# Kernel tuning notes

Hardware: AMD Instinct MI355X
Metric: run time of the kernel (lower is better)

The kernel has to match this reference:

```python
import jax, jax.numpy as jnp
import numpy as np

B, C, H, W = 4, 64, 64, 64
CQK = C // 4  # query/key channels = in_dim // 4


def setup_inputs() -> dict:
    key = jax.random.key(0)
    ks = jax.random.split(key, 9)
    s = 0.05
    return {
        "x": jax.random.normal(ks[0], (B, C, H, W), jnp.float32),
        "x_RGB": jax.random.normal(ks[1], (B, C, H, W), jnp.float32),
        "Wq": jax.random.normal(ks[2], (CQK, C), jnp.float32) * s,  # 1x1 conv weight
        "bq": jax.random.normal(ks[3], (CQK,), jnp.float32) * s,
        "Wk": jax.random.normal(ks[4], (CQK, C), jnp.float32) * s,
        "bk": jax.random.normal(ks[5], (CQK,), jnp.float32) * s,
        "Wv": jax.random.normal(ks[6], (C, C), jnp.float32) * s,
        "bv": jax.random.normal(ks[7], (C,), jnp.float32) * s,
        "lam": jnp.zeros((1,), jnp.float32) + 0.5,  # nn.Parameter init is 0; use 0.5 so output depends on attention
    }


def reference(x, x_RGB, Wq, bq, Wk, bk, Wv, bv, lam):
    b, c, h, w = x.shape
    n = h * w
    xf = x.reshape(b, c, n)          # B,C,N
    xr = x_RGB.reshape(b, c, n)      # B,C,N
    # 1x1 convs are channel matmuls
    q = jnp.einsum('oc,bcn->bno', Wq, xr) + bq            # B,N,Cqk  (permuted query)
    k = jnp.einsum('oc,bcn->bon', Wk, xf) + bk[:, None]   # B,Cqk,N
    v = jnp.einsum('oc,bcn->bon', Wv, xf) + bv[:, None]   # B,C,N
    energy = jnp.einsum('bio,boj->bij', q, k)             # B,N,N
    attention = jax.nn.softmax(energy, axis=-1)
    # out[b,c,i] = sum_j V[b,c,j] * attention[b,i,j]
    out = jnp.einsum('bcj,bij->bci', v, attention)        # B,C,N
    out = out.reshape(b, c, h, w)
    return lam[0] * out + x
```

## Files before the change

### kernel.cpp

```cpp
#include <hip/hip_runtime.h>
#include <hip/hip_bf16.h>
#include <math.h>

#define B_   4
#define C_   64
#define N_   4096
#define L2E  1.4426950408889634f

typedef __attribute__((ext_vector_type(8)))  short bf16x8;
typedef __attribute__((ext_vector_type(4)))  float f32x4;
typedef __attribute__((ext_vector_type(16))) float f32x16;
typedef __attribute__((ext_vector_type(4)))  uint  uint4v;

#define MFMA16(a,b,c) __builtin_amdgcn_mfma_f32_16x16x32_bf16(a,b,c,0,0,0)
#define MFMA32(a,b,c) __builtin_amdgcn_mfma_f32_32x32x16_bf16(a,b,c,0,0,0)

static __device__ inline ushort f2bf(float f) {
    __hip_bfloat16 h = __float2bfloat16(f);
    return *reinterpret_cast<ushort*>(&h);
}
static __device__ inline uint packbf(float a, float b) {
    return (uint)f2bf(a) | ((uint)f2bf(b) << 16);
}
static __device__ inline uint cvtpk(float lo, float hi) {
    uint r;
    asm("v_cvt_pk_bf16_f32 %0, %1, %2" : "=v"(r) : "v"(lo), "v"(hi));
    return r;
}
static __device__ inline void plswap(uint &a, uint &b) {
    asm("v_permlane32_swap_b32 %0, %1" : "+v"(a), "+v"(b));
}
static __device__ inline float tmax16(const f32x16 &s) {
    float a0 = fmaxf(s[0], s[1]),  a1 = fmaxf(s[2], s[3]);
    float a2 = fmaxf(s[4], s[5]),  a3 = fmaxf(s[6], s[7]);
    float a4 = fmaxf(s[8], s[9]),  a5 = fmaxf(s[10], s[11]);
    float a6 = fmaxf(s[12], s[13]), a7 = fmaxf(s[14], s[15]);
    a0 = fmaxf(a0, a1); a2 = fmaxf(a2, a3); a4 = fmaxf(a4, a5); a6 = fmaxf(a6, a7);
    return fmaxf(fmaxf(a0, a2), fmaxf(a4, a6));
}
static __device__ inline float tsum16(const f32x16 &s) {
    float a0 = s[0] + s[1],  a1 = s[2] + s[3];
    float a2 = s[4] + s[5],  a3 = s[6] + s[7];
    float a4 = s[8] + s[9],  a5 = s[10] + s[11];
    float a6 = s[12] + s[13], a7 = s[14] + s[15];
    a0 += a1; a2 += a3; a4 += a5; a6 += a7;
    return (a0 + a2) + (a4 + a6);
}

__global__ __launch_bounds__(256) void qkv_mfma(
    const float* __restrict__ x, const float* __restrict__ xrgb,
    const float* __restrict__ Wq, const float* __restrict__ bq,
    const float* __restrict__ Wk, const float* __restrict__ bk,
    const float* __restrict__ Wv, const float* __restrict__ bv,
    ushort* __restrict__ Qo, ushort* __restrict__ Ko, ushort* __restrict__ Vo)
{
    __shared__ float BLs[96];
    __shared__ float OP[2][96][33];

    const int t = threadIdx.x, b = blockIdx.y, n0 = blockIdx.x * 32;
    const int w = t >> 6, lane = t & 63, li = lane & 15, g = lane >> 4;
    const int pw = w & 1, cw = w >> 1;

    const int n = n0 + pw * 16 + li;
    const int c0 = cw * 32 + g * 8;
    const float* xb = x    + ((size_t)b * C_ + c0) * N_ + n;
    const float* rb = xrgb + ((size_t)b * C_ + c0) * N_ + n;
    float fx[8], fr[8];
    #pragma unroll
    for (int r = 0; r < 8; ++r) { fx[r] = xb[(size_t)r * N_]; fr[r] = rb[(size_t)r * N_]; }

    float wf[6][8];
    #pragma unroll
    for (int ot = 0; ot < 6; ++ot) {
        const float* wsrc;
        if (ot == 0)      wsrc = Wq + li * 64 + c0;
        else if (ot == 1) wsrc = Wk + li * 64 + c0;
        else              wsrc = Wv + ((ot - 2) * 16 + li) * 64 + c0;
        const float4 a = *(const float4*)(wsrc);
        const float4 c = *(const float4*)(wsrc + 4);
        wf[ot][0] = a.x; wf[ot][1] = a.y; wf[ot][2] = a.z; wf[ot][3] = a.w;
        wf[ot][4] = c.x; wf[ot][5] = c.y; wf[ot][6] = c.z; wf[ot][7] = c.w;
    }

    if (t < 96)
        BLs[t] = (t < 16) ? bq[t] * L2E : (t < 32 ? bk[t - 16] : bv[t - 32]);

    bf16x8 bxf, brf;
    #pragma unroll
    for (int r = 0; r < 8; ++r) {
        bxf[r] = (short)f2bf(fx[r]);
        brf[r] = (short)f2bf(fr[r]);
    }

    const f32x4 cz = {0.f, 0.f, 0.f, 0.f};
    #pragma unroll
    for (int ot = 0; ot < 6; ++ot) {
        bf16x8 wa;
        const float s = (ot == 0) ? L2E : 1.0f;
        #pragma unroll
        for (int r = 0; r < 8; ++r) wa[r] = (short)f2bf(wf[ot][r] * s);
        const f32x4 acc = MFMA16(wa, (ot == 0 ? brf : bxf), cz);
        #pragma unroll
        for (int r = 0; r < 4; ++r)
            OP[cw][ot * 16 + g * 4 + r][pw * 16 + li] = acc[r];
    }
    __syncthreads();

    {
        const int p = t >> 3, cp = t & 7;
        const float q0 = OP[0][cp * 2][p]     + OP[1][cp * 2][p]     + BLs[cp * 2];
        const float q1 = OP[0][cp * 2 + 1][p] + OP[1][cp * 2 + 1][p] + BLs[cp * 2 + 1];
        *(uint*)&Qo[(size_t)(b * N_ + n0 + p) * 16 + cp * 2] = packbf(q0, q1);
        const float k0 = OP[0][16 + cp * 2][p]     + OP[1][16 + cp * 2][p]     + BLs[16 + cp * 2];
        const float k1 = OP[0][16 + cp * 2 + 1][p] + OP[1][16 + cp * 2 + 1][p] + BLs[16 + cp * 2 + 1];
        *(uint*)&Ko[(size_t)(b * N_ + n0 + p) * 16 + cp * 2] = packbf(k0, k1);
    }
    {
        const int ch = t >> 2, po = (t & 3) * 8;
        const float bs = BLs[32 + ch];
        uint4 o;
        #pragma unroll
        for (int e = 0; e < 4; ++e) {
            const float v0 = OP[0][32 + ch][po + 2 * e]     + OP[1][32 + ch][po + 2 * e]     + bs;
            const float v1 = OP[0][32 + ch][po + 2 * e + 1] + OP[1][32 + ch][po + 2 * e + 1] + bs;
            ((uint*)&o)[e] = packbf(v0, v1);
        }
        const size_t jt = (size_t)b * (N_ / 16) + ((n0 + po) >> 4);
        *(uint4*)&Vo[(jt * 64 + ch) * 16 + (po & 8)] = o;
    }
}

#define JG_   8
#define OTP   36
#define SMEM_FL (73728 + 1056 + 1056 + 128)

__global__ __launch_bounds__(512, 4) void flash32(
    const ushort* __restrict__ Qg, const ushort* __restrict__ Kg,
    const ushort* __restrict__ VT, const float* __restrict__ x,
    const float* __restrict__ lam, float* __restrict__ out)
{
    __shared__ __align__(16) char smem[SMEM_FL];
    float*  OT = (float*)smem;
    float*  MC = (float*)(smem + 73728);
    float*  LC = (float*)(smem + 73728 + 1056);
    float*  IV = (float*)(smem + 73728 + 2112);

    const int t = threadIdx.x, w = t >> 6, lane = t & 63;
    const int l31 = lane & 31, h = lane >> 5;

    const int wg = blockIdx.x;
    const int b  = (wg & 7) >> 1;
    const int it = ((wg >> 3) << 1) | (wg & 1);
    const int i0 = it * 32;

    const bf16x8 qf = *(const bf16x8*)(Qg + ((size_t)(b * N_ + i0 + l31)) * 16 + h * 8);

    const size_t jbase = (size_t)w * (N_ / JG_);
    const ushort* kp = Kg + ((size_t)(b * N_) + jbase + l31) * 16 + h * 8;
    const ushort* vt = VT + (((size_t)b * (N_ / 16) + jbase / 16) * 64 + l31) * 16 + h * 8;

    f32x16 acc0, acc1, z16;
    #pragma unroll
    for (int i = 0; i < 16; ++i) { acc0[i] = 0.f; acc1[i] = 0.f; z16[i] = 0.f; }
    float m_run = -1e30f, l_loc = 0.f;

    #pragma unroll 1
    for (int it8 = 0; it8 < 8; ++it8) {
        const int j0 = it8 * 64;

        const bf16x8 kf0 = *(const bf16x8*)(kp + (size_t)(j0) * 16);
        const bf16x8 kf1 = *(const bf16x8*)(kp + (size_t)(j0 + 32) * 16);
        f32x16 st0 = MFMA32(kf0, qf, z16);
        f32x16 st1 = MFMA32(kf1, qf, z16);

        float m_c = fmaxf(tmax16(st0), tmax16(st1));
        m_c = fmaxf(m_c, __shfl_xor(m_c, 32));
        if (__any(m_c > m_run + 8.f)) {
            const float m_new = fmaxf(m_run, m_c);
            const float sc = exp2f(m_run - m_new);
            l_loc *= sc;
            #pragma unroll
            for (int i = 0; i < 16; ++i) { acc0[i] *= sc; acc1[i] *= sc; }
            m_run = m_new;
        }
        #pragma unroll
        for (int i = 0; i < 16; ++i) st0[i] = exp2f(st0[i] - m_run);
        #pragma unroll
        for (int i = 0; i < 16; ++i) st1[i] = exp2f(st1[i] - m_run);
        l_loc += tsum16(st0) + tsum16(st1);

        uint A0 = cvtpk(st0[0],  st0[1]),  A1 = cvtpk(st0[2],  st0[3]);
        uint B0 = cvtpk(st0[4],  st0[5]),  B1 = cvtpk(st0[6],  st0[7]);
        uint C0 = cvtpk(st0[8],  st0[9]),  C1 = cvtpk(st0[10], st0[11]);
        uint D0 = cvtpk(st0[12], st0[13]), D1 = cvtpk(st0[14], st0[15]);
        plswap(A0, B0); plswap(A1, B1); plswap(C0, D0); plswap(C1, D1);
        uint E0 = cvtpk(st1[0],  st1[1]),  E1 = cvtpk(st1[2],  st1[3]);
        uint F0 = cvtpk(st1[4],  st1[5]),  F1 = cvtpk(st1[6],  st1[7]);
        uint G0 = cvtpk(st1[8],  st1[9]),  G1 = cvtpk(st1[10], st1[11]);
        uint H0 = cvtpk(st1[12], st1[13]), H1 = cvtpk(st1[14], st1[15]);
        plswap(E0, F0); plswap(E1, F1); plswap(G0, H0); plswap(G1, H1);
        uint4v u0 = {A0, A1, B0, B1}, u1 = {C0, C1, D0, D1};
        uint4v u2 = {E0, E1, F0, F1}, u3 = {G0, G1, H0, H1};
        const bf16x8 pf0 = __builtin_bit_cast(bf16x8, u0);
        const bf16x8 pf1 = __builtin_bit_cast(bf16x8, u1);
        const bf16x8 pf2 = __builtin_bit_cast(bf16x8, u2);
        const bf16x8 pf3 = __builtin_bit_cast(bf16x8, u3);

        const ushort* vtj = vt + (size_t)(j0 >> 4) * 1024;
        const bf16x8 va0 = *(const bf16x8*)(vtj);
        const bf16x8 va1 = *(const bf16x8*)(vtj + 1024);
        const bf16x8 va2 = *(const bf16x8*)(vtj + 2048);
        const bf16x8 va3 = *(const bf16x8*)(vtj + 3072);
        acc0 = MFMA32(va0, pf0, acc0);
        acc0 = MFMA32(va1, pf1, acc0);
        acc0 = MFMA32(va2, pf2, acc0);
        acc0 = MFMA32(va3, pf3, acc0);
        const bf16x8 vb0 = *(const bf16x8*)(vtj + 512);
        const bf16x8 vb1 = *(const bf16x8*)(vtj + 1536);
        const bf16x8 vb2 = *(const bf16x8*)(vtj + 2560);
        const bf16x8 vb3 = *(const bf16x8*)(vtj + 3584);
        acc1 = MFMA32(vb0, pf0, acc1);
        acc1 = MFMA32(vb1, pf1, acc1);
        acc1 = MFMA32(vb2, pf2, acc1);
        acc1 = MFMA32(vb3, pf3, acc1);
    }
    const float l_run = l_loc + __shfl_xor(l_loc, 32);

    if (h == 0) { MC[w * 33 + l31] = m_run; LC[w * 33 + l31] = l_run; }
    __syncthreads();

    float mp[8];
    #pragma unroll
    for (int p = 0; p < 8; ++p) mp[p] = MC[p * 33 + l31];
    float ms = mp[0];
    #pragma unroll
    for (int p = 1; p < 8; ++p) ms = fmaxf(ms, mp[p]);
    float lsum = 0.f, wt_own = 0.f;
    #pragma unroll
    for (int p = 0; p < 8; ++p) {
        const float wt = exp2f(mp[p] - ms);
        lsum += wt * LC[p * 33 + l31];
        if (p == w) wt_own = wt;
    }
    if (w == 0 && h == 0) IV[l31] = lam[0] / lsum;

    #pragma unroll
    for (int r = 0; r < 16; ++r) {
        const int c = (r & 3) + 8 * (r >> 2) + 4 * h;
        OT[(w * 64 + c) * OTP + l31]      = acc0[r] * wt_own;
        OT[(w * 64 + c + 32) * OTP + l31] = acc1[r] * wt_own;
    }
    __syncthreads();

    {
        const int c = t >> 3, sg = t & 7;
        f32x4 o = {0.f, 0.f, 0.f, 0.f};
        #pragma unroll
        for (int p = 0; p < 8; ++p) {
            const f32x4 v = *(const f32x4*)&OT[(p * 64 + c) * OTP + sg * 4];
            o[0] += v[0]; o[1] += v[1]; o[2] += v[2]; o[3] += v[3];
        }
        const size_t off = ((size_t)b * C_ + c) * N_ + i0 + sg * 4;
        const float4 xv = *(const float4*)(x + off);
        float4 res;
        res.x = o[0] * IV[sg * 4 + 0] + xv.x;
        res.y = o[1] * IV[sg * 4 + 1] + xv.y;
        res.z = o[2] * IV[sg * 4 + 2] + xv.z;
        res.w = o[3] * IV[sg * 4 + 3] + xv.w;
        *(float4*)(out + off) = res;
    }
}

extern "C" void kernel_launch(void* const* d_in, const int* in_sizes, int n_in,
                              void* d_out, int out_size, void* d_ws, size_t ws_size,
                              hipStream_t stream)
{
    (void)in_sizes; (void)n_in; (void)out_size; (void)ws_size;
    const float* x    = (const float*)d_in[0];
    const float* xrgb = (const float*)d_in[1];
    const float* Wq   = (const float*)d_in[2];
    const float* bq   = (const float*)d_in[3];
    const float* Wk   = (const float*)d_in[4];
    const float* bk   = (const float*)d_in[5];
    const float* Wv   = (const float*)d_in[6];
    const float* bv   = (const float*)d_in[7];
    const float* lam  = (const float*)d_in[8];
    float* out = (float*)d_out;

    ushort* Qw = (ushort*)d_ws;
    ushort* Kw = Qw + (size_t)B_ * N_ * 16;
    ushort* Vw = Kw + (size_t)B_ * N_ * 16;

    qkv_mfma<<<dim3(N_ / 32, B_), 256, 0, stream>>>(
        x, xrgb, Wq, bq, Wk, bk, Wv, bv, Qw, Kw, Vw);

    flash32<<<dim3(512), 512, 0, stream>>>(
        Qw, Kw, Vw, x, lam, out);
}
```

Measured before the change: 36.80 us.

## Drop LDS reduction in QKV projection and shrink flash loop tile to 32 keys

The projection kernel now has each wave accumulate over both channel halves with chained MFMAs and write bias-added bf16 results straight to global memory. This removes the shared-memory partial-sum buffers and the block barrier. The V output becomes scattered 2-byte stores instead of 16-byte vector stores. The attention kernel processes 32 keys per iteration instead of 64, which halves live score registers and interleaves the two accumulator chains, at the cost of twice as many iterations and more frequent max checks.

```diff
diff --git a/kernel.cpp b/kernel.cpp
--- a/kernel.cpp
+++ b/kernel.cpp
@@ -54,79 +54,66 @@
     const float* __restrict__ Wv, const float* __restrict__ bv,
     ushort* __restrict__ Qo, ushort* __restrict__ Ko, ushort* __restrict__ Vo)
 {
-    __shared__ float BLs[96];
-    __shared__ float OP[2][96][33];
-
     const int t = threadIdx.x, b = blockIdx.y, n0 = blockIdx.x * 32;
     const int w = t >> 6, lane = t & 63, li = lane & 15, g = lane >> 4;
-    const int pw = w & 1, cw = w >> 1;
-
-    const int n = n0 + pw * 16 + li;
-    const int c0 = cw * 32 + g * 8;
-    const float* xb = x    + ((size_t)b * C_ + c0) * N_ + n;
-    const float* rb = xrgb + ((size_t)b * C_ + c0) * N_ + n;
-    float fx[8], fr[8];
-    #pragma unroll
-    for (int r = 0; r < 8; ++r) { fx[r] = xb[(size_t)r * N_]; fr[r] = rb[(size_t)r * N_]; }
-
-    float wf[6][8];
-    #pragma unroll
-    for (int ot = 0; ot < 6; ++ot) {
+    const int pw = w & 1, oh = w >> 1;
+
+    const int px = n0 + pw * 16 + li;
+
+    bf16x8 bxf[2], brf[2];
+    #pragma unroll
+    for (int kk = 0; kk < 2; ++kk) {
+        const int c0 = kk * 32 + g * 8;
+        const float* xb = x + ((size_t)b * C_ + c0) * N_ + px;
+        #pragma unroll
+        for (int r = 0; r < 8; ++r) bxf[kk][r] = (short)f2bf(xb[(size_t)r * N_]);
+        if (oh == 0) {
+            const float* rb = xrgb + ((size_t)b * C_ + c0) * N_ + px;
+            #pragma unroll
+            for (int r = 0; r < 8; ++r) brf[kk][r] = (short)f2bf(rb[(size_t)r * N_]);
+        }
+    }
+
+    const f32x4 cz = {0.f, 0.f, 0.f, 0.f};
+    #pragma unroll
+    for (int j = 0; j < 3; ++j) {
+        const int ot = oh * 3 + j;
         const float* wsrc;
-        if (ot == 0)      wsrc = Wq + li * 64 + c0;
-        else if (ot == 1) wsrc = Wk + li * 64 + c0;
-        else              wsrc = Wv + ((ot - 2) * 16 + li) * 64 + c0;
-        const float4 a = *(const float4*)(wsrc);
-        const float4 c = *(const float4*)(wsrc + 4);
-        wf[ot][0] = a.x; wf[ot][1] = a.y; wf[ot][2] = a.z; wf[ot][3] = a.w;
-        wf[ot][4] = c.x; wf[ot][5] = c.y; wf[ot][6] = c.z; wf[ot][7] = c.w;
-    }
-
-    if (t < 96)
-        BLs[t] = (t < 16) ? bq[t] * L2E : (t < 32 ? bk[t - 16] : bv[t - 32]);
-
-    bf16x8 bxf, brf;
-    #pragma unroll
-    for (int r = 0; r < 8; ++r) {
-        bxf[r] = (short)f2bf(fx[r]);
-        brf[r] = (short)f2bf(fr[r]);
-    }
-
-    const f32x4 cz = {0.f, 0.f, 0.f, 0.f};
-    #pragma unroll
-    for (int ot = 0; ot < 6; ++ot) {
-        bf16x8 wa;
+        const float* bsrc;
+        if (ot == 0)      { wsrc = Wq + li * 64;              bsrc = bq; }
+        else if (ot == 1) { wsrc = Wk + li * 64;              bsrc = bk; }
+        else              { wsrc = Wv + ((ot - 2) * 16 + li) * 64; bsrc = bv + (ot - 2) * 16; }
         const float s = (ot == 0) ? L2E : 1.0f;
-        #pragma unroll
-        for (int r = 0; r < 8; ++r) wa[r] = (short)f2bf(wf[ot][r] * s);
-        const f32x4 acc = MFMA16(wa, (ot == 0 ? brf : bxf), cz);
-        #pragma unroll
-        for (int r = 0; r < 4; ++r)
-            OP[cw][ot * 16 + g * 4 + r][pw * 16 + li] = acc[r];
-    }
-    __syncthreads();
-
-    {
-        const int p = t >> 3, cp = t & 7;
-        const float q0 = OP[0][cp * 2][p]     + OP[1][cp * 2][p]     + BLs[cp * 2];
-        const float q1 = OP[0][cp * 2 + 1][p] + OP[1][cp * 2 + 1][p] + BLs[cp * 2 + 1];
-        *(uint*)&Qo[(size_t)(b * N_ + n0 + p) * 16 + cp * 2] = packbf(q0, q1);
-        const float k0 = OP[0][16 + cp * 2][p]     + OP[1][16 + cp * 2][p]     + BLs[16 + cp * 2];
-        const float k1 = OP[0][16 + cp * 2 + 1][p] + OP[1][16 + cp * 2 + 1][p] + BLs[16 + cp * 2 + 1];
-        *(uint*)&Ko[(size_t)(b * N_ + n0 + p) * 16 + cp * 2] = packbf(k0, k1);
-    }
-    {
-        const int ch = t >> 2, po = (t & 3) * 8;
-        const float bs = BLs[32 + ch];
-        uint4 o;
-        #pragma unroll
-        for (int e = 0; e < 4; ++e) {
-            const float v0 = OP[0][32 + ch][po + 2 * e]     + OP[1][32 + ch][po + 2 * e]     + bs;
-            const float v1 = OP[0][32 + ch][po + 2 * e + 1] + OP[1][32 + ch][po + 2 * e + 1] + bs;
-            ((uint*)&o)[e] = packbf(v0, v1);
-        }
-        const size_t jt = (size_t)b * (N_ / 16) + ((n0 + po) >> 4);
-        *(uint4*)&Vo[(jt * 64 + ch) * 16 + (po & 8)] = o;
+
+        f32x4 acc = cz;
+        #pragma unroll
+        for (int kk = 0; kk < 2; ++kk) {
+            const int c0 = kk * 32 + g * 8;
+            const float4 a  = *(const float4*)(wsrc + c0);
+            const float4 c4 = *(const float4*)(wsrc + c0 + 4);
+            bf16x8 wa;
+            wa[0] = (short)f2bf(a.x * s);  wa[1] = (short)f2bf(a.y * s);
+            wa[2] = (short)f2bf(a.z * s);  wa[3] = (short)f2bf(a.w * s);
+            wa[4] = (short)f2bf(c4.x * s); wa[5] = (short)f2bf(c4.y * s);
+            wa[6] = (short)f2bf(c4.z * s); wa[7] = (short)f2bf(c4.w * s);
+            acc = MFMA16(wa, (ot == 0 ? brf[kk] : bxf[kk]), acc);
+        }
+        const float b0 = bsrc[g * 4 + 0] * s, b1 = bsrc[g * 4 + 1] * s;
+        const float b2 = bsrc[g * 4 + 2] * s, b3 = bsrc[g * 4 + 3] * s;
+        if (ot < 2) {
+            uint2 pwd;
+            pwd.x = packbf(acc[0] + b0, acc[1] + b1);
+            pwd.y = packbf(acc[2] + b2, acc[3] + b3);
+            ushort* dst = (ot == 0 ? Qo : Ko) + (size_t)(b * N_ + px) * 16 + g * 4;
+            *(uint2*)dst = pwd;
+        } else {
+            const size_t base = (((size_t)b * (N_ / 16) + (px >> 4)) * 64
+                                 + (ot - 2) * 16 + g * 4) * 16 + (px & 15);
+            Vo[base]      = f2bf(acc[0] + b0);
+            Vo[base + 16] = f2bf(acc[1] + b1);
+            Vo[base + 32] = f2bf(acc[2] + b2);
+            Vo[base + 48] = f2bf(acc[3] + b3);
+        }
     }
 }
 
@@ -165,15 +152,11 @@
     float m_run = -1e30f, l_loc = 0.f;
 
     #pragma unroll 1
-    for (int it8 = 0; it8 < 8; ++it8) {
-        const int j0 = it8 * 64;
-
-        const bf16x8 kf0 = *(const bf16x8*)(kp + (size_t)(j0) * 16);
-        const bf16x8 kf1 = *(const bf16x8*)(kp + (size_t)(j0 + 32) * 16);
-        f32x16 st0 = MFMA32(kf0, qf, z16);
-        f32x16 st1 = MFMA32(kf1, qf, z16);
-
-        float m_c = fmaxf(tmax16(st0), tmax16(st1));
+    for (int jt = 0; jt < 16; ++jt) {
+        const bf16x8 kf = *(const bf16x8*)(kp + (size_t)(jt * 32) * 16);
+        f32x16 st = MFMA32(kf, qf, z16);
+
+        float m_c = tmax16(st);
         m_c = fmaxf(m_c, __shfl_xor(m_c, 32));
         if (__any(m_c > m_run + 8.f)) {
             const float m_new = fmaxf(m_run, m_c);
@@ -183,46 +166,29 @@
             for (int i = 0; i < 16; ++i) { acc0[i] *= sc; acc1[i] *= sc; }
             m_run = m_new;
         }
-        #pragma unroll
-        for (int i = 0; i < 16; ++i) st0[i] = exp2f(st0[i] - m_run);
-        #pragma unroll
-        for (int i = 0; i < 16; ++i) st1[i] = exp2f(st1[i] - m_run);
-        l_loc += tsum16(st0) + tsum16(st1);
-
-        uint A0 = cvtpk(st0[0],  st0[1]),  A1 = cvtpk(st0[2],  st0[3]);
-        uint B0 = cvtpk(st0[4],  st0[5]),  B1 = cvtpk(st0[6],  st0[7]);
-        uint C0 = cvtpk(st0[8],  st0[9]),  C1 = cvtpk(st0[10], st0[11]);
-        uint D0 = cvtpk(st0[12], st0[13]), D1 = cvtpk(st0[14], st0[15]);
+
+        #pragma unroll
+        for (int i = 0; i < 16; ++i) st[i] = exp2f(st[i] - m_run);
+        l_loc += tsum16(st);
+
+        uint A0 = cvtpk(st[0],  st[1]),  A1 = cvtpk(st[2],  st[3]);
+        uint B0 = cvtpk(st[4],  st[5]),  B1 = cvtpk(st[6],  st[7]);
+        uint C0 = cvtpk(st[8],  st[9]),  C1 = cvtpk(st[10], st[11]);
+        uint D0 = cvtpk(st[12], st[13]), D1 = cvtpk(st[14], st[15]);
         plswap(A0, B0); plswap(A1, B1); plswap(C0, D0); plswap(C1, D1);
-        uint E0 = cvtpk(st1[0],  st1[1]),  E1 = cvtpk(st1[2],  st1[3]);
-        uint F0 = cvtpk(st1[4],  st1[5]),  F1 = cvtpk(st1[6],  st1[7]);
-        uint G0 = cvtpk(st1[8],  st1[9]),  G1 = cvtpk(st1[10], st1[11]);
-        uint H0 = cvtpk(st1[12], st1[13]), H1 = cvtpk(st1[14], st1[15]);
-        plswap(E0, F0); plswap(E1, F1); plswap(G0, H0); plswap(G1, H1);
         uint4v u0 = {A0, A1, B0, B1}, u1 = {C0, C1, D0, D1};
-        uint4v u2 = {E0, E1, F0, F1}, u3 = {G0, G1, H0, H1};
         const bf16x8 pf0 = __builtin_bit_cast(bf16x8, u0);
         const bf16x8 pf1 = __builtin_bit_cast(bf16x8, u1);
-        const bf16x8 pf2 = __builtin_bit_cast(bf16x8, u2);
-        const bf16x8 pf3 = __builtin_bit_cast(bf16x8, u3);
-
-        const ushort* vtj = vt + (size_t)(j0 >> 4) * 1024;
+
+        const ushort* vtj = vt + (size_t)jt * 2048;
         const bf16x8 va0 = *(const bf16x8*)(vtj);
+        const bf16x8 vb0 = *(const bf16x8*)(vtj + 512);
         const bf16x8 va1 = *(const bf16x8*)(vtj + 1024);
-        const bf16x8 va2 = *(const bf16x8*)(vtj + 2048);
-        const bf16x8 va3 = *(const bf16x8*)(vtj + 3072);
+        const bf16x8 vb1 = *(const bf16x8*)(vtj + 1536);
         acc0 = MFMA32(va0, pf0, acc0);
+        acc1 = MFMA32(vb0, pf0, acc1);
         acc0 = MFMA32(va1, pf1, acc0);
-        acc0 = MFMA32(va2, pf2, acc0);
-        acc0 = MFMA32(va3, pf3, acc0);
-        const bf16x8 vb0 = *(const bf16x8*)(vtj + 512);
-        const bf16x8 vb1 = *(const bf16x8*)(vtj + 1536);
-        const bf16x8 vb2 = *(const bf16x8*)(vtj + 2560);
-        const bf16x8 vb3 = *(const bf16x8*)(vtj + 3584);
-        acc1 = MFMA32(vb0, pf0, acc1);
         acc1 = MFMA32(vb1, pf1, acc1);
-        acc1 = MFMA32(vb2, pf2, acc1);
-        acc1 = MFMA32(vb3, pf3, acc1);
     }
     const float l_run = l_loc + __shfl_xor(l_loc, 32);
 
```

New measurement: 38.41 us. +4.4%, slower.
